# Kernel optimization log

Measured on AMD Instinct MI355X. Metric: run time of the kernel, lower is better.

## Reference

```python
import jax, jax.numpy as jnp
import numpy as np

EMBEDDING_DIM = 256
CODEBOOK_SIZE = 1024
COMMITMENT_COST = 0.25


def setup_inputs() -> dict:
    key = jax.random.key(0)
    k1, k2 = jax.random.split(key)
    inputs = jax.random.normal(k1, (16, 4096, EMBEDDING_DIM), dtype=jnp.float32)
    embeddings = jax.random.normal(k2, (EMBEDDING_DIM, CODEBOOK_SIZE), dtype=jnp.float32)
    return {"inputs": inputs, "embeddings": embeddings}


def reference(inputs, embeddings):
    # inputs: [B, T, D]; embeddings: [D, K]
    D = embeddings.shape[0]
    K = embeddings.shape[1]
    flat = inputs.reshape(-1, D)  # [N, D]

    sim = flat @ embeddings
    dists = (jnp.sum(flat * flat, axis=1, keepdims=True)
             + jnp.sum(embeddings * embeddings, axis=0)
             - 2.0 * sim)
    flat_idx = jnp.argmin(dists, axis=1)  # [N]

    encodings = jax.nn.one_hot(flat_idx, K, dtype=jnp.float32)  # [N, K]
    encoding_indices = flat_idx.reshape(inputs.shape[:-1])  # [B, T]

    # embedding lookup: gather rows of embeddings^T -> [B, T, D]
    quantized = jnp.take(embeddings.T, encoding_indices, axis=0)

    e_latent_loss = jnp.mean(jnp.square(jax.lax.stop_gradient(quantized) - inputs))
    q_latent_loss = jnp.mean(jnp.square(quantized - jax.lax.stop_gradient(inputs)))
    loss = q_latent_loss + COMMITMENT_COST * e_latent_loss

    # straight-through estimator
    quantized_st = inputs + jax.lax.stop_gradient(quantized - inputs)

    return quantized_st, encodings, encoding_indices, loss
```

## Files before the change

kernel.cpp:

```cpp
#include <hip/hip_runtime.h>

#define N_ROWS 65536
#define DIM    256
#define KCB    1024

#define Q_OFF    0
#define ENC_OFF  (N_ROWS * DIM)
#define IDX_OFF  (ENC_OFF + N_ROWS * KCB)
#define LOSS_OFF (IDX_OFF + N_ROWS)

#define ET_OFF   (ENC_OFF + 0)
#define NRM_OFF  (ENC_OFF + 262144)
#define IDXI_OFF (ENC_OFF + 263168)
#define PART_OFF (ENC_OFF + 328704)
#define AMB_OFF  (ENC_OFF + 345088)
#define PMIN_OFF (ENC_OFF + 524288)
#define A2_OFF   (ENC_OFF + 4718592)
#define BST_OFF  (ENC_OFF + 21495808)

#define TAU 0.05f

typedef short  bf16x8 __attribute__((ext_vector_type(8)));
typedef float  f32x4  __attribute__((ext_vector_type(4)));
typedef unsigned short u16x8 __attribute__((ext_vector_type(8)));
#define AS1 __attribute__((address_space(1)))
#define AS3 __attribute__((address_space(3)))

__device__ inline unsigned short f2bf(float x) {
    unsigned u = __float_as_uint(x);
    return (unsigned short)((u + 0x7FFFu + ((u >> 16) & 1u)) >> 16);
}
__device__ inline float bf2f(unsigned short b) {
    return __uint_as_float(((unsigned)b) << 16);
}

__global__ __launch_bounds__(256)
void vq_prep_a(const float* __restrict__ X, float* __restrict__ out) {
    unsigned short* A2 = (unsigned short*)(out + A2_OFF);
    int gid = blockIdx.x * 256 + threadIdx.x;
    int row = gid >> 5;
    int d0  = (gid & 31) * 8;
    const float* xp = X + (size_t)row * DIM + d0;
    float4 v0 = *(const float4*)xp;
    float4 v1 = *(const float4*)(xp + 4);
    float xv[8] = {v0.x, v0.y, v0.z, v0.w, v1.x, v1.y, v1.z, v1.w};
    u16x8 h, l;
#pragma unroll
    for (int i = 0; i < 8; ++i) {
        unsigned short hb = f2bf(xv[i]);
        h[i] = hb;
        l[i] = f2bf(xv[i] - bf2f(hb));
    }
    *(u16x8*)(A2 + (size_t)row * 512 + d0) = h;
    *(u16x8*)(A2 + (size_t)row * 512 + 256 + d0) = l;
}

__global__ __launch_bounds__(64)
void vq_prep_b(const float* __restrict__ E, float* __restrict__ out) {
    float* ET  = out + ET_OFF;
    float* nrm = out + NRM_OFF;
    unsigned short* B2 = (unsigned short*)(out + BST_OFF);
    const int k = blockIdx.x, t = threadIdx.x;
    float v[4]; float s = 0.f;
    ushort4 hb, lb;
#pragma unroll
    for (int i = 0; i < 4; ++i) {
        float e = E[(size_t)(t * 4 + i) * KCB + k];
        v[i] = e; s += e * e;
        unsigned short h = f2bf(e);
        ((unsigned short*)&hb)[i] = h;
        ((unsigned short*)&lb)[i] = f2bf(e - bf2f(h));
    }
    *(float4*)(ET + (size_t)k * DIM + t * 4) = *(float4*)v;
    *(ushort4*)(B2 + (size_t)k * 512 + t * 4) = hb;
    *(ushort4*)(B2 + (size_t)k * 512 + 256 + t * 4) = lb;
#pragma unroll
    for (int off = 32; off >= 1; off >>= 1) s += __shfl_xor(s, off);
    if (t == 0) nrm[k] = s;
    if (k == 0 && t == 0) ((int*)(out + AMB_OFF))[0] = 0;
}

__global__ __launch_bounds__(256, 3)
void vq_gemm(float* __restrict__ out) {
    __shared__ short lds[24576];
    const unsigned short* A2 = (const unsigned short*)(out + A2_OFF);
    const unsigned short* B2 = (const unsigned short*)(out + BST_OFF);
    const float* nrm = out + NRM_OFF;
    float4* pmin = (float4*)(out + PMIN_OFF);

    const int orig = blockIdx.x;
    const int mapped = (orig & 7) * 512 + (orig >> 3);
    const int rb = mapped >> 3, cb = mapped & 7;
    const int row0 = rb * 128, col0 = cb * 128;

    const int tid = threadIdx.x;
    const int lane = tid & 63, l15 = lane & 15, lhi = lane >> 4;
    const int w = tid >> 6, wr = w >> 1, wc = w & 1;
    const int swz = (l15 & 7) * 8;

    f32x4 acc[4][4];
#pragma unroll
    for (int i = 0; i < 4; ++i)
#pragma unroll
        for (int j = 0; j < 4; ++j) acc[i][j] = (f32x4){0.f, 0.f, 0.f, 0.f};

    const int sr   = tid >> 3;
    const int sksw = ((tid & 7) ^ ((tid >> 3) & 7)) * 8;
    const int wofs = (tid & 192) * 16;

#define STAGE4(SRC, R0, KOFF, LDSB)                                           \
    _Pragma("unroll")                                                         \
    for (int i = 0; i < 4; ++i) {                                             \
        __builtin_amdgcn_global_load_lds(                                     \
            (const AS1 unsigned*)((SRC) + (size_t)((R0) + i * 32 + sr) * 512  \
                                  + (KOFF) + sksw),                           \
            (AS3 unsigned*)((char*)lds + (LDSB) + i * 4096 + wofs), 16, 0, 0);\
    }

    for (int kr = 0; kr < 4; ++kr) {
        __syncthreads();
        STAGE4(A2, row0, kr * 64, 0);
        STAGE4(B2, col0, kr * 64, 16384);
        STAGE4(B2, col0, 256 + kr * 64, 32768);
        asm volatile("s_waitcnt vmcnt(0)" ::: "memory");
        __syncthreads();
#pragma unroll
        for (int kk = 0; kk < 2; ++kk) {
            const int cofs = (kk * 32 + lhi * 8) ^ swz;
            bf16x8 af[4], bh[4], bl[4];
#pragma unroll
            for (int mi = 0; mi < 4; ++mi)
                af[mi] = *(const bf16x8*)&lds[(wr * 64 + mi * 16 + l15) * 64 + cofs];
#pragma unroll
            for (int ni = 0; ni < 4; ++ni) {
                bh[ni] = *(const bf16x8*)&lds[8192 + (wc * 64 + ni * 16 + l15) * 64 + cofs];
                bl[ni] = *(const bf16x8*)&lds[16384 + (wc * 64 + ni * 16 + l15) * 64 + cofs];
            }
#pragma unroll
            for (int mi = 0; mi < 4; ++mi)
#pragma unroll
                for (int ni = 0; ni < 4; ++ni)
                    acc[mi][ni] = __builtin_amdgcn_mfma_f32_16x16x32_bf16(
                        af[mi], bh[ni], acc[mi][ni], 0, 0, 0);
#pragma unroll
            for (int mi = 0; mi < 4; ++mi)
#pragma unroll
                for (int ni = 0; ni < 4; ++ni)
                    acc[mi][ni] = __builtin_amdgcn_mfma_f32_16x16x32_bf16(
                        af[mi], bl[ni], acc[mi][ni], 0, 0, 0);
        }
    }
    for (int kr = 0; kr < 4; ++kr) {
        __syncthreads();
        STAGE4(A2, row0, 256 + kr * 64, 0);
        STAGE4(B2, col0, kr * 64, 16384);
        asm volatile("s_waitcnt vmcnt(0)" ::: "memory");
        __syncthreads();
#pragma unroll
        for (int kk = 0; kk < 2; ++kk) {
            const int cofs = (kk * 32 + lhi * 8) ^ swz;
            bf16x8 af[4], bh[4];
#pragma unroll
            for (int mi = 0; mi < 4; ++mi)
                af[mi] = *(const bf16x8*)&lds[(wr * 64 + mi * 16 + l15) * 64 + cofs];
#pragma unroll
            for (int ni = 0; ni < 4; ++ni)
                bh[ni] = *(const bf16x8*)&lds[8192 + (wc * 64 + ni * 16 + l15) * 64 + cofs];
#pragma unroll
            for (int mi = 0; mi < 4; ++mi)
#pragma unroll
                for (int ni = 0; ni < 4; ++ni)
                    acc[mi][ni] = __builtin_amdgcn_mfma_f32_16x16x32_bf16(
                        af[mi], bh[ni], acc[mi][ni], 0, 0, 0);
        }
    }
#undef STAGE4

    float nv[4];
#pragma unroll
    for (int ni = 0; ni < 4; ++ni) nv[ni] = nrm[col0 + wc * 64 + ni * 16 + l15];
#pragma unroll
    for (int mi = 0; mi < 4; ++mi)
#pragma unroll
        for (int j = 0; j < 4; ++j) {
            float a = 3.4e38f, b = 3.4e38f; int ia = 0;
#pragma unroll
            for (int ni = 0; ni < 4; ++ni) {
                float dist = fmaf(-2.f, acc[mi][ni][j], nv[ni]);
                int col = col0 + wc * 64 + ni * 16 + l15;
                if (dist < a) { b = a; a = dist; ia = col; }
                else if (dist < b) b = dist;
            }
#pragma unroll
            for (int off = 1; off < 16; off <<= 1) {
                float oa = __shfl_xor(a, off);
                float ob = __shfl_xor(b, off);
                int   oi = __shfl_xor(ia, off);
                if (oa < a || (oa == a && oi < ia)) { b = fminf(a, ob); a = oa; ia = oi; }
                else b = fminf(b, oa);
            }
            if (l15 == 0) {
                int grow = row0 + wr * 64 + mi * 16 + lhi * 4 + j;
                float4 pv;
                pv.x = a; pv.y = b; pv.z = __int_as_float(ia); pv.w = 0.f;
                pmin[(size_t)grow * 16 + cb * 2 + wc] = pv;
            }
        }
}

__global__ __launch_bounds__(256)
void vq_combine(float* __restrict__ out) {
    const float4* pmin = (const float4*)(out + PMIN_OFF);
    int* idxi = (int*)(out + IDXI_OFF);
    int* amb  = (int*)(out + AMB_OFF);
    const int row = blockIdx.x * 256 + threadIdx.x;
    float a = 3.4e38f, b = 3.4e38f; int ia = 0;
#pragma unroll
    for (int s = 0; s < 16; ++s) {
        float4 p = pmin[(size_t)row * 16 + s];
        int oi = __float_as_int(p.z);
        if (p.x < a || (p.x == a && oi < ia)) { b = fminf(a, p.y); a = p.x; ia = oi; }
        else b = fminf(b, p.x);
    }
    idxi[row] = ia;
    if (b - a < TAU) {
        int pos = atomicAdd(amb, 1);
        if (pos < 65536) amb[1 + pos] = row;
    }
}

__global__ __launch_bounds__(256)
void vq_rescore(const float* __restrict__ X, float* __restrict__ out) {
    __shared__ float xs[4][256];
    const float* ET  = out + ET_OFF;
    const float* nrm = out + NRM_OFF;
    const int* amb = (const int*)(out + AMB_OFF);
    int* idxi = (int*)(out + IDXI_OFF);
    const int wid = threadIdx.x >> 6, lane = threadIdx.x & 63;
    int count = amb[0]; if (count > 65536) count = 65536;
    for (int it = blockIdx.x * 4 + wid; it < count; it += gridDim.x * 4) {
        const int row = amb[1 + it];
        *(float4*)&xs[wid][lane * 4] = *(const float4*)(X + (size_t)row * DIM + lane * 4);
        float best = 3.4e38f; int bi = 0;
        for (int cc = 0; cc < 16; ++cc) {
            const int code = cc * 64 + lane;
            const float* ep = ET + (size_t)code * DIM;
            float acc = 0.f;
#pragma unroll
            for (int d = 0; d < 256; d += 4) {
                float4 ev = *(const float4*)(ep + d);
                acc = fmaf(xs[wid][d],     ev.x, acc);
                acc = fmaf(xs[wid][d + 1], ev.y, acc);
                acc = fmaf(xs[wid][d + 2], ev.z, acc);
                acc = fmaf(xs[wid][d + 3], ev.w, acc);
            }
            float dist = fmaf(-2.f, acc, nrm[code]);
            if (dist < best) { best = dist; bi = code; }
        }
#pragma unroll
        for (int off = 1; off < 64; off <<= 1) {
            float ov = __shfl_xor(best, off);
            int   oi = __shfl_xor(bi, off);
            if (ov < best || (ov == best && oi < bi)) { best = ov; bi = oi; }
        }
        if (lane == 0) idxi[row] = bi;
    }
}

__global__ __launch_bounds__(256)
void vq_outputs(const float* __restrict__ X, float* __restrict__ out) {
    const float* ET  = out + ET_OFF;
    const int*   idx = (const int*)(out + IDXI_OFF);
    float*       part = out + PART_OFF;
    __shared__ float red[4];
    const int row  = blockIdx.x * 4 + (threadIdx.x >> 6);
    const int lane = threadIdx.x & 63;
    const int id   = idx[row];
    float4 e = *(const float4*)(ET + (size_t)id * DIM + lane * 4);
    float4 x = *(const float4*)(X + (size_t)row * DIM + lane * 4);
    float dx = e.x - x.x, dy = e.y - x.y, dz = e.z - x.z, dw = e.w - x.w;
    float4 q;
    q.x = x.x + dx; q.y = x.y + dy; q.z = x.z + dz; q.w = x.w + dw;
    *(float4*)(out + Q_OFF + (size_t)row * DIM + lane * 4) = q;
    float s = dx * dx + dy * dy + dz * dz + dw * dw;
#pragma unroll
    for (int off = 32; off >= 1; off >>= 1) s += __shfl_xor(s, off);
    if (lane == 0) {
        red[threadIdx.x >> 6] = s;
        out[IDX_OFF + row] = (float)id;
    }
    __syncthreads();
    if (threadIdx.x == 0) part[blockIdx.x] = red[0] + red[1] + red[2] + red[3];
}

__global__ __launch_bounds__(256)
void vq_loss(float* __restrict__ out) {
    const float* part = out + PART_OFF;
    __shared__ double red[256];
    const int tid = threadIdx.x;
    double s = 0.0;
    for (int i = tid; i < 16384; i += 256) s += (double)part[i];
    red[tid] = s;
    __syncthreads();
    for (int off = 128; off > 0; off >>= 1) {
        if (tid < off) red[tid] += red[tid + off];
        __syncthreads();
    }
    if (tid == 0)
        out[LOSS_OFF] = (float)(1.25 * red[0] / (double)((size_t)N_ROWS * DIM));
}

__global__ __launch_bounds__(256)
void vq_encodings(float* __restrict__ out) {
    const float* idxf = out + IDX_OFF;
    float4* enc4 = (float4*)(out + ENC_OFF);
    const size_t total4 = (size_t)N_ROWS * KCB / 4;
    const size_t stride = (size_t)gridDim.x * blockDim.x;
    for (size_t g = (size_t)blockIdx.x * blockDim.x + threadIdx.x; g < total4; g += stride) {
        int n  = (int)(g >> 8);
        int c0 = ((int)g & 255) * 4;
        int r  = (int)idxf[n] - c0;
        float4 v;
        v.x = (r == 0) ? 1.f : 0.f;
        v.y = (r == 1) ? 1.f : 0.f;
        v.z = (r == 2) ? 1.f : 0.f;
        v.w = (r == 3) ? 1.f : 0.f;
        enc4[g] = v;
    }
}

extern "C" void kernel_launch(void* const* d_in, const int* in_sizes, int n_in,
                              void* d_out, int out_size, void* d_ws, size_t ws_size,
                              hipStream_t stream) {
    const float* X = (const float*)d_in[0];
    const float* E = (const float*)d_in[1];
    float* out = (float*)d_out;

    vq_prep_a   <<<8192, 256, 0, stream>>>(X, out);
    vq_prep_b   <<<1024,  64, 0, stream>>>(E, out);
    vq_gemm     <<<4096, 256, 0, stream>>>(out);
    vq_combine  <<<256,  256, 0, stream>>>(out);
    vq_rescore  <<<1024, 256, 0, stream>>>(X, out);
    vq_outputs  <<<16384, 256, 0, stream>>>(X, out);
    vq_loss     <<<1,    256, 0, stream>>>(out);
    vq_encodings<<<2048, 256, 0, stream>>>(out);
}
```

Before: 709.1 us.

## Track top-2 indices and rescore only near-tie candidates instead of full codebook

The GEMM epilogue now keeps the second-best index as well as the best, and the combine kernel gathers every code within TAU of the best across the 16 partials. Ambiguous rows with at most 6 candidates (and no second-best inside the window) get an exact fp32 rescoring of just those candidates. Other ambiguous rows fall back to the full 1024-code rescoring. The GEMM also reuses one register array for the high and low B fragments, which lowers register pressure. The risks are that candidates can be missed when a partial's third-best lies inside the window (handled by the ok flag), that the fixed capacities are finite, and that one thread scanning 256 floats gives uncoalesced loads.

```diff
diff --git a/kernel.cpp b/kernel.cpp
--- a/kernel.cpp
+++ b/kernel.cpp
@@ -19,6 +19,8 @@
 #define BST_OFF  (ENC_OFF + 21495808)
 
 #define TAU 0.05f
+#define MAXCAND 20000
+#define MAXFB   16000
 
 typedef short  bf16x8 __attribute__((ext_vector_type(8)));
 typedef float  f32x4  __attribute__((ext_vector_type(4)));
@@ -77,7 +79,7 @@
 #pragma unroll
     for (int off = 32; off >= 1; off >>= 1) s += __shfl_xor(s, off);
     if (t == 0) nrm[k] = s;
-    if (k == 0 && t == 0) ((int*)(out + AMB_OFF))[0] = 0;
+    if (k == 0 && t == 0) { int* a = (int*)(out + AMB_OFF); a[0] = 0; a[1] = 0; }
 }
 
 __global__ __launch_bounds__(256, 3)
@@ -127,27 +129,28 @@
 #pragma unroll
         for (int kk = 0; kk < 2; ++kk) {
             const int cofs = (kk * 32 + lhi * 8) ^ swz;
-            bf16x8 af[4], bh[4], bl[4];
+            bf16x8 af[4], bf[4];
 #pragma unroll
             for (int mi = 0; mi < 4; ++mi)
                 af[mi] = *(const bf16x8*)&lds[(wr * 64 + mi * 16 + l15) * 64 + cofs];
 #pragma unroll
-            for (int ni = 0; ni < 4; ++ni) {
-                bh[ni] = *(const bf16x8*)&lds[8192 + (wc * 64 + ni * 16 + l15) * 64 + cofs];
-                bl[ni] = *(const bf16x8*)&lds[16384 + (wc * 64 + ni * 16 + l15) * 64 + cofs];
-            }
+            for (int ni = 0; ni < 4; ++ni)
+                bf[ni] = *(const bf16x8*)&lds[8192 + (wc * 64 + ni * 16 + l15) * 64 + cofs];
 #pragma unroll
             for (int mi = 0; mi < 4; ++mi)
 #pragma unroll
                 for (int ni = 0; ni < 4; ++ni)
                     acc[mi][ni] = __builtin_amdgcn_mfma_f32_16x16x32_bf16(
-                        af[mi], bh[ni], acc[mi][ni], 0, 0, 0);
+                        af[mi], bf[ni], acc[mi][ni], 0, 0, 0);
+#pragma unroll
+            for (int ni = 0; ni < 4; ++ni)
+                bf[ni] = *(const bf16x8*)&lds[16384 + (wc * 64 + ni * 16 + l15) * 64 + cofs];
 #pragma unroll
             for (int mi = 0; mi < 4; ++mi)
 #pragma unroll
                 for (int ni = 0; ni < 4; ++ni)
                     acc[mi][ni] = __builtin_amdgcn_mfma_f32_16x16x32_bf16(
-                        af[mi], bl[ni], acc[mi][ni], 0, 0, 0);
+                        af[mi], bf[ni], acc[mi][ni], 0, 0, 0);
         }
     }
     for (int kr = 0; kr < 4; ++kr) {
@@ -159,19 +162,19 @@
 #pragma unroll
         for (int kk = 0; kk < 2; ++kk) {
             const int cofs = (kk * 32 + lhi * 8) ^ swz;
-            bf16x8 af[4], bh[4];
+            bf16x8 af[4], bf[4];
 #pragma unroll
             for (int mi = 0; mi < 4; ++mi)
                 af[mi] = *(const bf16x8*)&lds[(wr * 64 + mi * 16 + l15) * 64 + cofs];
 #pragma unroll
             for (int ni = 0; ni < 4; ++ni)
-                bh[ni] = *(const bf16x8*)&lds[8192 + (wc * 64 + ni * 16 + l15) * 64 + cofs];
+                bf[ni] = *(const bf16x8*)&lds[8192 + (wc * 64 + ni * 16 + l15) * 64 + cofs];
 #pragma unroll
             for (int mi = 0; mi < 4; ++mi)
 #pragma unroll
                 for (int ni = 0; ni < 4; ++ni)
                     acc[mi][ni] = __builtin_amdgcn_mfma_f32_16x16x32_bf16(
-                        af[mi], bh[ni], acc[mi][ni], 0, 0, 0);
+                        af[mi], bf[ni], acc[mi][ni], 0, 0, 0);
         }
     }
 #undef STAGE4
@@ -183,26 +186,31 @@
     for (int mi = 0; mi < 4; ++mi)
 #pragma unroll
         for (int j = 0; j < 4; ++j) {
-            float a = 3.4e38f, b = 3.4e38f; int ia = 0;
+            float a = 3.4e38f, b = 3.4e38f; int ia = 0, ib = 0;
 #pragma unroll
             for (int ni = 0; ni < 4; ++ni) {
                 float dist = fmaf(-2.f, acc[mi][ni][j], nv[ni]);
                 int col = col0 + wc * 64 + ni * 16 + l15;
-                if (dist < a) { b = a; a = dist; ia = col; }
-                else if (dist < b) b = dist;
+                if (dist < a) { b = a; ib = ia; a = dist; ia = col; }
+                else if (dist < b) { b = dist; ib = col; }
             }
 #pragma unroll
             for (int off = 1; off < 16; off <<= 1) {
-                float oa = __shfl_xor(a, off);
-                float ob = __shfl_xor(b, off);
-                int   oi = __shfl_xor(ia, off);
-                if (oa < a || (oa == a && oi < ia)) { b = fminf(a, ob); a = oa; ia = oi; }
-                else b = fminf(b, oa);
+                float oa = __shfl_xor(a, off), ob = __shfl_xor(b, off);
+                int   oi = __shfl_xor(ia, off), oj = __shfl_xor(ib, off);
+                if (oa < a || (oa == a && oi < ia)) {
+                    if (a < ob || (a == ob && ia < oj)) { b = a; ib = ia; }
+                    else { b = ob; ib = oj; }
+                    a = oa; ia = oi;
+                } else {
+                    if (oa < b || (oa == b && oi < ib)) { b = oa; ib = oi; }
+                }
             }
             if (l15 == 0) {
                 int grow = row0 + wr * 64 + mi * 16 + lhi * 4 + j;
                 float4 pv;
-                pv.x = a; pv.y = b; pv.z = __int_as_float(ia); pv.w = 0.f;
+                pv.x = a; pv.y = __int_as_float(ia);
+                pv.z = b; pv.w = __int_as_float(ib);
                 pmin[(size_t)grow * 16 + cb * 2 + wc] = pv;
             }
         }
@@ -213,33 +221,81 @@
     const float4* pmin = (const float4*)(out + PMIN_OFF);
     int* idxi = (int*)(out + IDXI_OFF);
     int* amb  = (int*)(out + AMB_OFF);
+    int* fb   = (int*)(out + PART_OFF);
     const int row = blockIdx.x * 256 + threadIdx.x;
+    float v1[16], v2[16]; int i1[16], i2[16];
     float a = 3.4e38f, b = 3.4e38f; int ia = 0;
 #pragma unroll
     for (int s = 0; s < 16; ++s) {
         float4 p = pmin[(size_t)row * 16 + s];
-        int oi = __float_as_int(p.z);
-        if (p.x < a || (p.x == a && oi < ia)) { b = fminf(a, p.y); a = p.x; ia = oi; }
-        else b = fminf(b, p.x);
+        v1[s] = p.x; i1[s] = __float_as_int(p.y);
+        v2[s] = p.z; i2[s] = __float_as_int(p.w);
+        if (v1[s] < a || (v1[s] == a && i1[s] < ia)) { b = fminf(a, v2[s]); a = v1[s]; ia = i1[s]; }
+        else b = fminf(b, v1[s]);
     }
     idxi[row] = ia;
     if (b - a < TAU) {
-        int pos = atomicAdd(amb, 1);
-        if (pos < 65536) amb[1 + pos] = row;
-    }
-}
-
-__global__ __launch_bounds__(256)
-void vq_rescore(const float* __restrict__ X, float* __restrict__ out) {
+        const float lim = a + TAU;
+        int cands[6]; int nc = 0; bool ok = true;
+#pragma unroll
+        for (int s = 0; s < 16; ++s) {
+            if (v1[s] < lim) { if (nc < 6) cands[nc] = i1[s]; ++nc; }
+            if (v2[s] < lim) { if (nc < 6) cands[nc] = i2[s]; ++nc; ok = false; }
+        }
+        if (ok && nc <= 6) {
+            int pos = atomicAdd(&amb[0], 1);
+            if (pos < MAXCAND) {
+                int* e = amb + 16 + pos * 8;
+                e[0] = row; e[1] = nc;
+#pragma unroll
+                for (int c = 0; c < 6; ++c) e[2 + c] = (c < nc) ? cands[c] : 0;
+            } else ok = false;
+        } else ok = false;
+        if (!ok) {
+            int pos = atomicAdd(&amb[1], 1);
+            if (pos < MAXFB) fb[pos] = row;
+        }
+    }
+}
+
+__global__ __launch_bounds__(256)
+void vq_rescore_cand(const float* __restrict__ X, float* __restrict__ out) {
+    const float* ET  = out + ET_OFF;
+    const float* nrm = out + NRM_OFF;
+    const int* amb = (const int*)(out + AMB_OFF);
+    int* idxi = (int*)(out + IDXI_OFF);
+    int count = amb[0]; if (count > MAXCAND) count = MAXCAND;
+    for (int it = blockIdx.x * 256 + threadIdx.x; it < count; it += gridDim.x * 256) {
+        const int* e = amb + 16 + it * 8;
+        const int row = e[0], nc = e[1];
+        const float* xp = X + (size_t)row * DIM;
+        float best = 3.4e38f; int bi = 0x7fffffff;
+        for (int c = 0; c < nc; ++c) {
+            const int code = e[2 + c];
+            const float* ep = ET + (size_t)code * DIM;
+            float acc = 0.f;
+#pragma unroll 8
+            for (int d = 0; d < 256; ++d)
+                acc = fmaf(xp[d], ep[d], acc);
+            float dist = fmaf(-2.f, acc, nrm[code]);
+            if (dist < best || (dist == best && code < bi)) { best = dist; bi = code; }
+        }
+        idxi[row] = bi;
+    }
+}
+
+__global__ __launch_bounds__(256)
+void vq_rescore_fb(const float* __restrict__ X, float* __restrict__ out) {
     __shared__ float xs[4][256];
     const float* ET  = out + ET_OFF;
     const float* nrm = out + NRM_OFF;
     const int* amb = (const int*)(out + AMB_OFF);
+    const int* fb  = (const int*)(out + PART_OFF);
     int* idxi = (int*)(out + IDXI_OFF);
     const int wid = threadIdx.x >> 6, lane = threadIdx.x & 63;
-    int count = amb[0]; if (count > 65536) count = 65536;
+    int count = amb[1]; if (count > MAXFB) count = MAXFB;
     for (int it = blockIdx.x * 4 + wid; it < count; it += gridDim.x * 4) {
-        const int row = amb[1 + it];
+        const int row = fb[it];
         *(float4*)&xs[wid][lane * 4] = *(const float4*)(X + (size_t)row * DIM + lane * 4);
         float best = 3.4e38f; int bi = 0;
         for (int cc = 0; cc < 16; ++cc) {
@@ -336,12 +392,13 @@
     const float* E = (const float*)d_in[1];
     float* out = (float*)d_out;
 
-    vq_prep_a   <<<8192, 256, 0, stream>>>(X, out);
-    vq_prep_b   <<<1024,  64, 0, stream>>>(E, out);
-    vq_gemm     <<<4096, 256, 0, stream>>>(out);
-    vq_combine  <<<256,  256, 0, stream>>>(out);
-    vq_rescore  <<<1024, 256, 0, stream>>>(X, out);
-    vq_outputs  <<<16384, 256, 0, stream>>>(X, out);
-    vq_loss     <<<1,    256, 0, stream>>>(out);
-    vq_encodings<<<2048, 256, 0, stream>>>(out);
-}
+    vq_prep_a      <<<8192, 256, 0, stream>>>(X, out);
+    vq_prep_b      <<<1024,  64, 0, stream>>>(E, out);
+    vq_gemm        <<<4096, 256, 0, stream>>>(out);
+    vq_combine     <<<256,  256, 0, stream>>>(out);
+    vq_rescore_cand<<<64,   256, 0, stream>>>(X, out);
+    vq_rescore_fb  <<<128,  256, 0, stream>>>(X, out);
+    vq_outputs     <<<16384, 256, 0, stream>>>(X, out);
+    vq_loss        <<<1,    256, 0, stream>>>(out);
+    vq_encodings   <<<2048, 256, 0, stream>>>(out);
+}
```

After: 755.7 us. +6.6%, slower.
